# Kernel tuning notes

Measured on AMD Instinct MI355X. Metric: run time of the kernel, lower is better.

## Reference

```python
import jax, jax.numpy as jnp
import numpy as np

K = 3  # spatial kernel size (TVConv_k_square == 9)


def setup_inputs() -> dict:
    key = jax.random.key(0)
    k1, k2 = jax.random.split(key)
    B, C, H, W = 8, 96, 128, 128
    x = jax.random.normal(k1, (B, C, H, W), dtype=jnp.float32)
    weight_maps = jax.random.normal(k2, (1, C, K, K, H, W), dtype=jnp.float32)
    return {"x": x, "weight_maps": weight_maps}


def reference(x, weight_maps):
    # Per-pixel spatially-varying 3x3 depthwise conv.
    B, C, H, W = x.shape
    xp = jnp.pad(x, ((0, 0), (0, 0), (1, 1), (1, 1)))  # zero pad, (B,C,H+2,W+2)
    # Gather the 9 shifted views (equivalent to the as_strided unfold, stride 1).
    patches = jnp.stack(
        [xp[:, :, i:i + H, j:j + W] for i in range(K) for j in range(K)], axis=2
    ).reshape(B, C, K, K, H, W)
    # Weighted sum over the 3x3 window per channel per pixel.
    out = (weight_maps * patches).sum(axis=(2, 3))  # (B,C,H,W)
    return out
```

## Files before the change

### kernel.cpp

```cpp
#include <hip/hip_runtime.h>
#include <hip/hip_bf16.h>


namespace {
constexpr int B = 8, C = 96, H = 128, W = 128;
constexpr int HW = H * W;
constexpr int W4 = W / 4;
}

__global__ __launch_bounds__(256) void tvconv_kernel(
    const float* __restrict__ x,
    const float* __restrict__ wm,
    float* __restrict__ out) {
  const int tid = blockIdx.x * blockDim.x + threadIdx.x;
  const int w4 = tid & (W4 - 1);
  const int h  = (tid >> 5) & (H - 1);
  const int c  = tid >> 12;
  if (c >= C) return;
  const int w = w4 * 4;

  float wt[3][3][4];
  const float* wp = wm + (size_t)c * 9 * HW + h * W + w;
  #pragma unroll
  for (int i = 0; i < 3; ++i) {
    #pragma unroll
    for (int j = 0; j < 3; ++j) {
      const float4 v = *reinterpret_cast<const float4*>(wp + (size_t)(i * 3 + j) * HW);
      wt[i][j][0] = v.x; wt[i][j][1] = v.y; wt[i][j][2] = v.z; wt[i][j][3] = v.w;
    }
  }

  #pragma unroll
  for (int b = 0; b < B; ++b) {
    const float* xb = x + ((size_t)b * C + c) * HW;
    float acc[4] = {0.f, 0.f, 0.f, 0.f};
    #pragma unroll
    for (int i = 0; i < 3; ++i) {
      const int hh = h + i - 1;
      if (hh < 0 || hh >= H) continue;
      const float* xr = xb + hh * W + w;
      const float4 ctr = *reinterpret_cast<const float4*>(xr);
      const float left  = (w > 0)     ? xr[-1] : 0.f;
      const float right = (w + 4 < W) ? xr[4]  : 0.f;
      const float xv[6] = {left, ctr.x, ctr.y, ctr.z, ctr.w, right};
      #pragma unroll
      for (int j = 0; j < 3; ++j) {
        #pragma unroll
        for (int k = 0; k < 4; ++k) {
          acc[k] += wt[i][j][k] * xv[k + j];
        }
      }
    }
    float4 o;
    o.x = acc[0]; o.y = acc[1]; o.z = acc[2]; o.w = acc[3];
    *reinterpret_cast<float4*>(out + ((size_t)b * C + c) * HW + h * W + w) = o;
  }
}

extern "C" void kernel_launch(void* const* d_in, const int* in_sizes, int n_in,
                              void* d_out, int out_size, void* d_ws, size_t ws_size,
                              hipStream_t stream) {
  const float* x  = (const float*)d_in[0];
  const float* wm = (const float*)d_in[1];
  float* out = (float*)d_out;

  const int total_threads = C * H * W4;
  const int block = 256;
  const int grid = (total_threads + block - 1) / block;
  tvconv_kernel<<<grid, block, 0, stream>>>(x, wm, out);
}
```

Measured before the change: 154.5 us.

## Split batch across grid-y, prefetch rows, use wave shuffles for halo

Each thread now handles 4 batches instead of 8, and the grid gains a second dimension over batch halves, doubling the number of threads. All three input rows for the 4 batches are loaded up front to increase memory-level parallelism. The left/right halo values come from neighboring lanes via shuffles instead of extra scalar global loads. Weight maps are now read once per batch half, adding some weight traffic.

```diff
diff --git a/kernel.cpp b/kernel.cpp
--- a/kernel.cpp
+++ b/kernel.cpp
@@ -8,52 +8,64 @@
 constexpr int W4 = W / 4;
 }
 
-__global__ __launch_bounds__(256) void tvconv_kernel(
+__global__ __launch_bounds__(256, 4) void tvconv_kernel(
     const float* __restrict__ x,
     const float* __restrict__ wm,
     float* __restrict__ out) {
-  const int tid = blockIdx.x * blockDim.x + threadIdx.x;
+  const int tid = blockIdx.x * 256 + threadIdx.x;
   const int w4 = tid & (W4 - 1);
   const int h  = (tid >> 5) & (H - 1);
   const int c  = tid >> 12;
-  if (c >= C) return;
-  const int w = w4 * 4;
+  const int w  = w4 * 4;
+  const int b0 = blockIdx.y * 4;
 
-  float wt[3][3][4];
+  float4 wt[9];
   const float* wp = wm + (size_t)c * 9 * HW + h * W + w;
-  #pragma unroll
-  for (int i = 0; i < 3; ++i) {
-    #pragma unroll
-    for (int j = 0; j < 3; ++j) {
-      const float4 v = *reinterpret_cast<const float4*>(wp + (size_t)(i * 3 + j) * HW);
-      wt[i][j][0] = v.x; wt[i][j][1] = v.y; wt[i][j][2] = v.z; wt[i][j][3] = v.w;
-    }
+#pragma unroll
+  for (int k = 0; k < 9; ++k) {
+    wt[k] = *reinterpret_cast<const float4*>(wp + (size_t)k * HW);
   }
 
-  #pragma unroll
-  for (int b = 0; b < B; ++b) {
-    const float* xb = x + ((size_t)b * C + c) * HW;
+  const bool hlo = (h > 0), hhi = (h < H - 1);
+  const float4 zero4 = make_float4(0.f, 0.f, 0.f, 0.f);
+  float4 xr[4][3];
+#pragma unroll
+  for (int bb = 0; bb < 4; ++bb) {
+    const float* xb = x + ((size_t)(b0 + bb) * C + c) * HW + h * W + w;
+    float4 up = zero4, dn = zero4;
+    if (hlo) up = *reinterpret_cast<const float4*>(xb - W);
+    const float4 mid = *reinterpret_cast<const float4*>(xb);
+    if (hhi) dn = *reinterpret_cast<const float4*>(xb + W);
+    xr[bb][0] = up; xr[bb][1] = mid; xr[bb][2] = dn;
+  }
+
+  const bool at_left  = (w4 == 0);
+  const bool at_right = (w4 == W4 - 1);
+#pragma unroll
+  for (int bb = 0; bb < 4; ++bb) {
     float acc[4] = {0.f, 0.f, 0.f, 0.f};
-    #pragma unroll
+#pragma unroll
     for (int i = 0; i < 3; ++i) {
-      const int hh = h + i - 1;
-      if (hh < 0 || hh >= H) continue;
-      const float* xr = xb + hh * W + w;
-      const float4 ctr = *reinterpret_cast<const float4*>(xr);
-      const float left  = (w > 0)     ? xr[-1] : 0.f;
-      const float right = (w + 4 < W) ? xr[4]  : 0.f;
+      const float4 ctr = xr[bb][i];
+      float left  = __shfl_up(ctr.w, 1);
+      float right = __shfl_down(ctr.x, 1);
+      if (at_left)  left  = 0.f;
+      if (at_right) right = 0.f;
       const float xv[6] = {left, ctr.x, ctr.y, ctr.z, ctr.w, right};
-      #pragma unroll
+#pragma unroll
       for (int j = 0; j < 3; ++j) {
-        #pragma unroll
+        const float4 wv = wt[i * 3 + j];
+        const float wa[4] = {wv.x, wv.y, wv.z, wv.w};
+#pragma unroll
         for (int k = 0; k < 4; ++k) {
-          acc[k] += wt[i][j][k] * xv[k + j];
+          acc[k] += wa[k] * xv[k + j];
         }
       }
     }
     float4 o;
     o.x = acc[0]; o.y = acc[1]; o.z = acc[2]; o.w = acc[3];
-    *reinterpret_cast<float4*>(out + ((size_t)b * C + c) * HW + h * W + w) = o;
+    *reinterpret_cast<float4*>(
+        out + ((size_t)(b0 + bb) * C + c) * HW + h * W + w) = o;
   }
 }
 
@@ -66,6 +78,6 @@
 
   const int total_threads = C * H * W4;
   const int block = 256;
-  const int grid = (total_threads + block - 1) / block;
-  tvconv_kernel<<<grid, block, 0, stream>>>(x, wm, out);
+  dim3 grid((total_threads + block - 1) / block, B / 4);
+  tvconv_kernel<<<grid, dim3(block, 1, 1), 0, stream>>>(x, wm, out);
 }
```

Measured after the change: 142.9 us. 1.08x faster.
